# Optimization experiments

Hardware: AMD Instinct MI355X
Metric: run time of the kernel (lower is better)

The kernel has to match this reference:

```python
import jax, jax.numpy as jnp
import numpy as np

D_MODEL = 1024
N_HEADS = 16
D_HEAD = D_MODEL // N_HEADS
RANK = 16
DECAY = 0.95
ALPHA_MAX = 0.05
BETA = 0.01


def setup_inputs() -> dict:
    key = jax.random.key(0)
    ks = jax.random.split(key, 9)
    B, T = 4, 2048
    s = 0.02  # init scale for weights
    return {
        "hidden_states": jax.random.normal(ks[0], (B, T, D_MODEL), jnp.float32),
        "m_gate": jax.random.uniform(ks[1], (B, T), jnp.float32),
        "alpha_scale": jax.random.uniform(ks[2], (B, T, N_HEADS), jnp.float32),
        "Wq": jax.random.normal(ks[3], (D_MODEL, D_MODEL), jnp.float32) * s,
        "Wk": jax.random.normal(ks[4], (D_MODEL, D_MODEL), jnp.float32) * s,
        "Wv": jax.random.normal(ks[5], (D_MODEL, D_MODEL), jnp.float32) * s,
        "Wo": jax.random.normal(ks[6], (D_MODEL, D_MODEL), jnp.float32) * s,
        "Wa": jax.random.normal(ks[7], (N_HEADS, D_MODEL), jnp.float32) * s,
        "ba": jnp.zeros((N_HEADS,), jnp.float32),
        "mix_logit": jnp.zeros((N_HEADS,), jnp.float32),
    }


def reference(hidden_states, m_gate, alpha_scale, Wq, Wk, Wv, Wo, Wa, ba, mix_logit):
    B, T, D = hidden_states.shape
    H, Dh, R = N_HEADS, D_HEAD, RANK
    # batched projections (Linear: x @ W.T), then split heads
    q = (hidden_states @ Wq.T).reshape(B, T, H, Dh)
    k = (hidden_states @ Wk.T).reshape(B, T, H, Dh)
    v = (hidden_states @ Wv.T).reshape(B, T, H, Dh)
    # alpha computed under torch.no_grad in the original -> stop_gradient
    alpha = jax.nn.sigmoid(hidden_states @ Wa.T + ba)  # [B,T,H]
    alpha = alpha * m_gate[..., None] * alpha_scale
    alpha = jnp.minimum(alpha, ALPHA_MAX)
    alpha = jax.lax.stop_gradient(alpha)

    inv_sqrt_dh = 1.0 / (Dh ** 0.5)

    def step(carry, xs):
        U, V = carry  # U: [B,H,Dh,R], V: [B,H,R,Dh]
        q_t, k_t, v_t, a_t = xs  # [B,H,Dh], [B,H,Dh], [B,H,Dh], [B,H]
        U = DECAY * U
        V = DECAY * V
        ku = jnp.einsum('bhd,bhdr->bhr', k_t, U)
        a = a_t[..., None, None]
        U = U + a * jnp.einsum('bhd,bhr->bhdr', k_t, ku)
        V = V + a * jnp.einsum('bhr,bhd->bhrd', ku, v_t)
        U = U - BETA * jnp.clip(U, -1.0, 1.0)
        V = V - BETA * jnp.clip(V, -1.0, 1.0)
        # whole fast-weight update is no_grad in the original
        U = jax.lax.stop_gradient(U)
        V = jax.lax.stop_gradient(V)
        q_norm = q_t * inv_sqrt_dh
        k_fast = jnp.einsum('bhdr,bhrd->bhd', U, V)  # [B,H,Dh]
        score_slow = jnp.sum(q_norm * k_t, axis=-1)  # [B,H]
        score_fast = jnp.sum(q_norm * k_fast, axis=-1)
        logits = jnp.stack([score_slow, score_fast], axis=-1) + mix_logit[None, :, None]
        mix = jax.nn.softmax(logits, axis=-1)  # [B,H,2]
        y = mix[..., 0:1] * v_t + mix[..., 1:2] * k_fast  # [B,H,Dh]
        return (U, V), y

    U0 = jnp.zeros((B, H, Dh, R), hidden_states.dtype)
    V0 = jnp.zeros((B, H, R, Dh), hidden_states.dtype)
    xs = (jnp.moveaxis(q, 1, 0), jnp.moveaxis(k, 1, 0),
          jnp.moveaxis(v, 1, 0), jnp.moveaxis(alpha, 1, 0))
    _, ys = jax.lax.scan(step, (U0, V0), xs)  # ys: [T,B,H,Dh]
    y = jnp.moveaxis(ys, 0, 1).reshape(B, T, D)
    return y @ Wo.T
```

## Files before the change

kernel.cpp:

```cpp
#include <hip/hip_runtime.h>
#include <hip/hip_bf16.h>
#include <stdint.h>

#define D_MODEL 1024
#define N_HEADS 16
#define D_HEAD  64
#define SEQ_T   2048
#define BATCH   4

typedef unsigned short u16;
typedef __bf16 bf16x8 __attribute__((ext_vector_type(8)));
typedef float  f32x4  __attribute__((ext_vector_type(4)));

#define NT 32
#define BUF 4096
#define QNT 32

__device__ __forceinline__ u16 f2bf(float x) {
  unsigned u = __float_as_uint(x);
  u += 0x7fffu + ((u >> 16) & 1u);
  return (u16)(u >> 16);
}
__device__ __forceinline__ unsigned pk2(float a, float b) {
  return (unsigned)f2bf(a) | ((unsigned)f2bf(b) << 16);
}
__device__ __forceinline__ unsigned scale2(unsigned p, float s) {
  float lo = __uint_as_float(p << 16) * s;
  float hi = __uint_as_float(p & 0xffff0000u) * s;
  unsigned r;
  asm("v_cvt_pk_bf16_f32 %0, %1, %2" : "=v"(r) : "v"(lo), "v"(hi));
  return r;
}
__device__ __forceinline__ void cp16(const u16* g, u16* l) {
  __builtin_amdgcn_global_load_lds(
      (const __attribute__((address_space(1))) unsigned int*)g,
      (__attribute__((address_space(3))) unsigned int*)l, 16, 0, 0);
}

__global__ __launch_bounds__(256) void cast_kernel(const float* __restrict__ hs,
                                                   const float* __restrict__ wq,
                                                   const float* __restrict__ wk,
                                                   const float* __restrict__ wv,
                                                   const float* __restrict__ wo,
                                                   u16* __restrict__ Xb,
                                                   u16* __restrict__ Wb) {
  int g = blockIdx.x * 256 + threadIdx.x;
  const float4* src; uint4* dst;
  if (g < (1 << 20)) {
    src = (const float4*)hs + 2 * (size_t)g;
    dst = (uint4*)Xb + g;
  } else {
    int j = g - (1 << 20);
    int R = j >> 7;
    int col8 = j & 127;
    const float* s;
    int srow;
    if (R < 2048) {
      int h = R >> 7, c = R & 127, jj = c >> 4, l = c & 15;
      srow = h * 64 + (jj >> 1) * 16 + l;
      s = (jj & 1) ? wk : wq;
    } else if (R < 3072) { s = wv; srow = R - 2048; }
    else                 { s = wo; srow = R - 3072; }
    src = (const float4*)s + (size_t)srow * 256 + col8 * 2;
    dst = (uint4*)Wb + (size_t)R * 128 + col8;
  }
  float4 lo = src[0], hi = src[1];
  uint4 o;
  o.x = pk2(lo.x, lo.y); o.y = pk2(lo.z, lo.w);
  o.z = pk2(hi.x, hi.y); o.w = pk2(hi.z, hi.w);
  *dst = o;
}

#define QVM(n) asm volatile("s_waitcnt vmcnt(" #n ")" ::: "memory")

__global__ __launch_bounds__(256, 2) void gemm_qkv_kernel(const u16* __restrict__ A,
                                                          const u16* __restrict__ B,
                                                          u16* __restrict__ Vb,
                                                          float* __restrict__ S) {
  __shared__ u16 Ls[36864];
  const int tid  = threadIdx.x;
  const int w    = tid >> 6;
  const int l    = tid & 63;
  const int quad = l >> 4;
  const int l16  = l & 15;
  const int wm   = (w >> 1) * 128;
  const int wn   = (w & 1) * 64;

  const int id  = blockIdx.y * 24 + blockIdx.x;
  const int id2 = (id & 7) * 96 + (id >> 3);
  const int bm  = id2 / 24;
  const int bn  = id2 % 24;

  const int srow = w * 16 + (l >> 2);
  const int schk = (l & 3) * 8;
  const u16* aS[4]; const u16* bS[2];
  #pragma unroll
  for (int r = 0; r < 4; ++r)
    aS[r] = A + (size_t)(bm * 256 + r * 64 + srow) * 1024 + schk;
  #pragma unroll
  for (int r = 0; r < 2; ++r)
    bS[r] = B + (size_t)(bn * 128 + r * 64 + srow) * 1024 + schk;
  u16* dA = Ls + w * 512 + l * 8;
  u16* dB = Ls + 24576 + w * 512 + l * 8;

  f32x4 acc[8][4];
  #pragma unroll
  for (int i = 0; i < 8; ++i)
    #pragma unroll
    for (int j = 0; j < 4; ++j) acc[i][j] = (f32x4){0.f, 0.f, 0.f, 0.f};

  #pragma unroll
  for (int r = 0; r < 4; ++r) cp16(aS[r] + 0 * 32, dA + 0 * 8192 + r * 2048);
  #pragma unroll
  for (int r = 0; r < 2; ++r) cp16(bS[r] + 0 * 32, dB + 0 * 4096 + r * 2048);
  #pragma unroll
  for (int r = 0; r < 4; ++r) cp16(aS[r] + 1 * 32, dA + 1 * 8192 + r * 2048);
  #pragma unroll
  for (int r = 0; r < 2; ++r) cp16(bS[r] + 1 * 32, dB + 1 * 4096 + r * 2048);
  QVM(6);
  __builtin_amdgcn_s_barrier();

  int rbuf = 0, sbuf = 2;
  #pragma unroll 1
  for (int t = 0; t < QNT; ++t) {
    if (t + 2 < QNT) {
      #pragma unroll
      for (int r = 0; r < 4; ++r)
        cp16(aS[r] + (t + 2) * 32, dA + sbuf * 8192 + r * 2048);
      #pragma unroll
      for (int r = 0; r < 2; ++r)
        cp16(bS[r] + (t + 2) * 32, dB + sbuf * 4096 + r * 2048);
    }
    const u16* Ar = Ls + rbuf * 8192;
    const u16* Br = Ls + 24576 + rbuf * 4096;
    bf16x8 af[8], bfr[4];
    #pragma unroll
    for (int i = 0; i < 8; ++i)
      af[i] = *(const bf16x8*)(Ar + (wm + i * 16 + l16) * 32 + quad * 8);
    #pragma unroll
    for (int j = 0; j < 4; ++j)
      bfr[j] = *(const bf16x8*)(Br + (wn + j * 16 + l16) * 32 + quad * 8);
    __builtin_amdgcn_s_setprio(1);
    #pragma unroll
    for (int i = 0; i < 8; ++i)
      #pragma unroll
      for (int j = 0; j < 4; ++j)
        acc[i][j] = __builtin_amdgcn_mfma_f32_16x16x32_bf16(af[i], bfr[j], acc[i][j], 0, 0, 0);
    __builtin_amdgcn_s_setprio(0);
    if (t + 2 < QNT) { QVM(6); } else { QVM(0); }
    __builtin_amdgcn_s_barrier();
    rbuf = (rbuf == 2) ? 0 : rbuf + 1;
    sbuf = (sbuf == 2) ? 0 : sbuf + 1;
  }

  if (bn < 16) {
    float part[8][4];
    #pragma unroll
    for (int i = 0; i < 8; ++i)
      #pragma unroll
      for (int e = 0; e < 4; ++e)
        part[i][e] = acc[i][0][e] * acc[i][1][e] + acc[i][2][e] * acc[i][3][e];
    #pragma unroll
    for (int m = 1; m <= 8; m <<= 1)
      #pragma unroll
      for (int i = 0; i < 8; ++i)
        #pragma unroll
        for (int e = 0; e < 4; ++e)
          part[i][e] += __shfl_xor(part[i][e], m);
    float* Sp = (float*)Ls;
    if (l16 == 0) {
      #pragma unroll
      for (int i = 0; i < 8; ++i)
        #pragma unroll
        for (int e = 0; e < 4; ++e)
          Sp[(wm + i * 16 + quad * 4 + e) * 2 + (w & 1)] = part[i][e];
    }
    __syncthreads();
    {
      int row = tid;
      float s = (Sp[row * 2] + Sp[row * 2 + 1]) * 0.125f;
      S[(size_t)(bm * 256 + row) * N_HEADS + bn] = 1.f / (1.f + __expf(-s));
    }
  } else {
    const int cb = (bn - 16) * 128;
    #pragma unroll
    for (int i = 0; i < 8; ++i)
      #pragma unroll
      for (int j = 0; j < 4; ++j)
        #pragma unroll
        for (int e = 0; e < 4; ++e) {
          int row = bm * 256 + wm + i * 16 + quad * 4 + e;
          int col = cb + wn + j * 16 + l16;
          Vb[(size_t)row * D_MODEL + col] = f2bf(acc[i][j][e]);
        }
  }
}

__global__ __launch_bounds__(256, 4) void gemm_out_kernel(const u16* __restrict__ A,
                                                          const u16* __restrict__ B,
                                                          const float* __restrict__ S,
                                                          float* __restrict__ C) {
  constexpr int K = D_MODEL, N = D_MODEL;
  __shared__ u16 As[2 * BUF];
  __shared__ u16 Bs[2 * BUF];
  const int tid  = threadIdx.x;
  const int lane = tid & 63;
  const int wave = tid >> 6;
  const int wm = (wave >> 1) * 64;
  const int wn = (wave & 1) * 64;
  const int quad = lane >> 4;
  const int l16  = lane & 15;
  const int rchunk = quad ^ ((l16 >> 1) & 3);

  const int id  = blockIdx.y * 8 + blockIdx.x;
  const int id2 = (id & 7) * 64 + (id >> 3);
  const int bm = (id2 >> 3) * 128;
  const int bn = (id2 & 7) * 128;

  const int lr = tid >> 2;
  const int lch = tid & 3;
  const int wch = lch ^ ((lr >> 1) & 3);
  const u16* Ap0 = A + (size_t)(bm + lr) * K + lch * 8;
  const u16* Ap1 = Ap0 + (size_t)64 * K;
  u16* Aw0 = As + lr * 32 + wch * 8;
  u16* Aw1 = Aw0 + 64 * 32;
  const float* Sp0 = S + (size_t)(bm + lr) * N_HEADS;
  const float* Sp1 = Sp0 + (size_t)64 * N_HEADS;

  const int srow = lane >> 2;
  const int gch  = (lane & 3) ^ ((lane >> 3) & 3);
  const u16* Bg0 = B + (size_t)(bn + wave * 16 + srow) * K + gch * 8;
  const u16* Bg1 = Bg0 + (size_t)64 * K;
  u16* Bl = Bs + wave * 16 * 32 + lane * 8;

  f32x4 acc[4][4];
  #pragma unroll
  for (int i = 0; i < 4; ++i)
    #pragma unroll
    for (int j = 0; j < 4; ++j) acc[i][j] = (f32x4){0.f, 0.f, 0.f, 0.f};

  uint4 a0 = *(const uint4*)Ap0;
  uint4 a1 = *(const uint4*)Ap1;
  float rs0 = Sp0[0], rs1 = Sp1[0];
  cp16(Bg0, Bl);           cp16(Bg1, Bl + 64 * 32);
  {
    uint4 w0, w1;
    w0.x = scale2(a0.x, rs0); w0.y = scale2(a0.y, rs0);
    w0.z = scale2(a0.z, rs0); w0.w = scale2(a0.w, rs0);
    w1.x = scale2(a1.x, rs1); w1.y = scale2(a1.y, rs1);
    w1.z = scale2(a1.z, rs1); w1.w = scale2(a1.w, rs1);
    *(uint4*)Aw0 = w0; *(uint4*)Aw1 = w1;
  }
  a0 = *(const uint4*)(Ap0 + 32);
  a1 = *(const uint4*)(Ap1 + 32);
  __syncthreads();

  #pragma unroll 2
  for (int t = 0; t < NT; ++t) {
    const int p = t & 1;
    const u16* Ar = As + p * BUF;
    const u16* Br = Bs + p * BUF;
    bf16x8 af[4], bfr[4];
    #pragma unroll
    for (int i = 0; i < 4; ++i)
      af[i] = *(const bf16x8*)(Ar + (wm + i * 16 + l16) * 32 + rchunk * 8);
    #pragma unroll
    for (int j = 0; j < 4; ++j)
      bfr[j] = *(const bf16x8*)(Br + (wn + j * 16 + l16) * 32 + rchunk * 8);
    if (t + 1 < NT) {
      const int q = (p ^ 1) * BUF;
      cp16(Bg0 + (t + 1) * 32, Bl + q);
      cp16(Bg1 + (t + 1) * 32, Bl + q + 64 * 32);
      uint4 w0, w1;
      w0.x = scale2(a0.x, rs0); w0.y = scale2(a0.y, rs0);
      w0.z = scale2(a0.z, rs0); w0.w = scale2(a0.w, rs0);
      w1.x = scale2(a1.x, rs1); w1.y = scale2(a1.y, rs1);
      w1.z = scale2(a1.z, rs1); w1.w = scale2(a1.w, rs1);
      *(uint4*)(Aw0 + q) = w0; *(uint4*)(Aw1 + q) = w1;
      if (t + 2 < NT) {
        const int o = (t + 2) * 32;
        a0 = *(const uint4*)(Ap0 + o);
        a1 = *(const uint4*)(Ap1 + o);
        rs0 = Sp0[(t + 2) >> 1];
        rs1 = Sp1[(t + 2) >> 1];
      }
    }
    #pragma unroll
    for (int i = 0; i < 4; ++i)
      #pragma unroll
      for (int j = 0; j < 4; ++j)
        acc[i][j] = __builtin_amdgcn_mfma_f32_16x16x32_bf16(af[i], bfr[j], acc[i][j], 0, 0, 0);
    __syncthreads();
  }

  #pragma unroll
  for (int i = 0; i < 4; ++i)
    #pragma unroll
    for (int j = 0; j < 4; ++j)
      #pragma unroll
      for (int e = 0; e < 4; ++e) {
        int row = bm + wm + i * 16 + quad * 4 + e;
        int col = bn + wn + j * 16 + l16;
        C[(size_t)row * N + col] = acc[i][j][e];
      }
}

extern "C" void kernel_launch(void* const* d_in, const int* in_sizes, int n_in,
                              void* d_out, int out_size, void* d_ws, size_t ws_size,
                              hipStream_t stream) {
  const float* hs = (const float*)d_in[0];
  const float* Wq = (const float*)d_in[3];
  const float* Wk = (const float*)d_in[4];
  const float* Wv = (const float*)d_in[5];
  const float* Wo = (const float*)d_in[6];

  char* ws = (char*)d_ws;
  u16*  Xb = (u16*)ws;
  u16*  Wb = (u16*)(ws + (16u << 20));
  u16*  Vb = (u16*)(ws + (24u << 20));
  float* Sb = (float*)(ws + (40u << 20));
  float* out = (float*)d_out;

  cast_kernel<<<6144, 256, 0, stream>>>(hs, Wq, Wk, Wv, Wo, Xb, Wb);
  gemm_qkv_kernel<<<dim3(24, 32), 256, 0, stream>>>(Xb, Wb, Vb, Sb);
  gemm_out_kernel<<<dim3(8, 64), 256, 0, stream>>>(
      Vb, Wb + (size_t)3072 * D_MODEL, Sb, out);
}
```

Baseline: 189.6 us.

## Fuse fp32-to-bf16 cast of hidden states into QKV GEMM A-tile staging

Stops pre-casting the 8M-element hidden_states to bf16 in a separate pass. The QKV GEMM now loads fp32 A tiles into registers, converts them with v_cvt_pk_bf16_f32, and writes them to LDS one stage behind the loads, while B still uses direct global-to-LDS copies. This removes a full read/write of the activation and shrinks the cast kernel, but the GEMM reads twice as many A bytes (each A tile is re-read by 24 column blocks), uses more registers, and adds LDS write work to the main loop.

New measurement: 201.4 us. +6.3%, slower.

```diff
diff --git a/kernel.cpp b/kernel.cpp
--- a/kernel.cpp
+++ b/kernel.cpp
@@ -24,12 +24,15 @@
 __device__ __forceinline__ unsigned pk2(float a, float b) {
   return (unsigned)f2bf(a) | ((unsigned)f2bf(b) << 16);
 }
+__device__ __forceinline__ unsigned cvtpk(float lo, float hi) {
+  unsigned r;
+  asm("v_cvt_pk_bf16_f32 %0, %1, %2" : "=v"(r) : "v"(lo), "v"(hi));
+  return r;
+}
 __device__ __forceinline__ unsigned scale2(unsigned p, float s) {
   float lo = __uint_as_float(p << 16) * s;
   float hi = __uint_as_float(p & 0xffff0000u) * s;
-  unsigned r;
-  asm("v_cvt_pk_bf16_f32 %0, %1, %2" : "=v"(r) : "v"(lo), "v"(hi));
-  return r;
+  return cvtpk(lo, hi);
 }
 __device__ __forceinline__ void cp16(const u16* g, u16* l) {
   __builtin_amdgcn_global_load_lds(
@@ -37,33 +40,24 @@
       (__attribute__((address_space(3))) unsigned int*)l, 16, 0, 0);
 }
 
-__global__ __launch_bounds__(256) void cast_kernel(const float* __restrict__ hs,
-                                                   const float* __restrict__ wq,
+__global__ __launch_bounds__(256) void cast_kernel(const float* __restrict__ wq,
                                                    const float* __restrict__ wk,
                                                    const float* __restrict__ wv,
                                                    const float* __restrict__ wo,
-                                                   u16* __restrict__ Xb,
                                                    u16* __restrict__ Wb) {
-  int g = blockIdx.x * 256 + threadIdx.x;
-  const float4* src; uint4* dst;
-  if (g < (1 << 20)) {
-    src = (const float4*)hs + 2 * (size_t)g;
-    dst = (uint4*)Xb + g;
-  } else {
-    int j = g - (1 << 20);
-    int R = j >> 7;
-    int col8 = j & 127;
-    const float* s;
-    int srow;
-    if (R < 2048) {
-      int h = R >> 7, c = R & 127, jj = c >> 4, l = c & 15;
-      srow = h * 64 + (jj >> 1) * 16 + l;
-      s = (jj & 1) ? wk : wq;
-    } else if (R < 3072) { s = wv; srow = R - 2048; }
-    else                 { s = wo; srow = R - 3072; }
-    src = (const float4*)s + (size_t)srow * 256 + col8 * 2;
-    dst = (uint4*)Wb + (size_t)R * 128 + col8;
-  }
+  int j = blockIdx.x * 256 + threadIdx.x;
+  int R = j >> 7;
+  int col8 = j & 127;
+  const float* s;
+  int srow;
+  if (R < 2048) {
+    int h = R >> 7, c = R & 127, jj = c >> 4, l = c & 15;
+    srow = h * 64 + (jj >> 1) * 16 + l;
+    s = (jj & 1) ? wk : wq;
+  } else if (R < 3072) { s = wv; srow = R - 2048; }
+  else                 { s = wo; srow = R - 3072; }
+  const float4* src = (const float4*)s + (size_t)srow * 256 + col8 * 2;
+  uint4* dst = (uint4*)Wb + (size_t)R * 128 + col8;
   float4 lo = src[0], hi = src[1];
   uint4 o;
   o.x = pk2(lo.x, lo.y); o.y = pk2(lo.z, lo.w);
@@ -73,7 +67,7 @@
 
 #define QVM(n) asm volatile("s_waitcnt vmcnt(" #n ")" ::: "memory")
 
-__global__ __launch_bounds__(256, 2) void gemm_qkv_kernel(const u16* __restrict__ A,
+__global__ __launch_bounds__(256, 2) void gemm_qkv_kernel(const float* __restrict__ A32,
                                                           const u16* __restrict__ B,
                                                           u16* __restrict__ Vb,
                                                           float* __restrict__ S) {
@@ -91,45 +85,69 @@
   const int bm  = id2 / 24;
   const int bn  = id2 % 24;
 
+  const int c4 = tid & 3;
+  const int r0 = tid >> 2;
+  const float* aG[4];
+  #pragma unroll
+  for (int u = 0; u < 4; ++u)
+    aG[u] = A32 + (size_t)(bm * 256 + u * 64 + r0) * 1024 + c4 * 8;
+  u16* aW = Ls + r0 * 32 + c4 * 8;
+
   const int srow = w * 16 + (l >> 2);
   const int schk = (l & 3) * 8;
-  const u16* aS[4]; const u16* bS[2];
-  #pragma unroll
-  for (int r = 0; r < 4; ++r)
-    aS[r] = A + (size_t)(bm * 256 + r * 64 + srow) * 1024 + schk;
+  const u16* bS[2];
   #pragma unroll
   for (int r = 0; r < 2; ++r)
     bS[r] = B + (size_t)(bn * 128 + r * 64 + srow) * 1024 + schk;
-  u16* dA = Ls + w * 512 + l * 8;
   u16* dB = Ls + 24576 + w * 512 + l * 8;
 
+  float4 av[4][2];
+
+#define STAGE_A_LOAD(t)                                                        \
+  do {                                                                         \
+    _Pragma("unroll") for (int _u = 0; _u < 4; ++_u) {                         \
+      av[_u][0] = *(const float4*)(aG[_u] + (t) * 32);                         \
+      av[_u][1] = *(const float4*)(aG[_u] + (t) * 32 + 4);                     \
+    }                                                                          \
+  } while (0)
+#define STAGE_A_WRITE(slot)                                                    \
+  do {                                                                         \
+    _Pragma("unroll") for (int _u = 0; _u < 4; ++_u) {                         \
+      uint4 _o;                                                                \
+      _o.x = cvtpk(av[_u][0].x, av[_u][0].y);                                  \
+      _o.y = cvtpk(av[_u][0].z, av[_u][0].w);                                  \
+      _o.z = cvtpk(av[_u][1].x, av[_u][1].y);                                  \
+      _o.w = cvtpk(av[_u][1].z, av[_u][1].w);                                  \
+      *(uint4*)(aW + (slot) * 8192 + _u * 2048) = _o;                          \
+    }                                                                          \
+  } while (0)
+#define STAGE_B(t, slot)                                                       \
+  do {                                                                         \
+    cp16(bS[0] + (t) * 32, dB + (slot) * 4096);                                \
+    cp16(bS[1] + (t) * 32, dB + (slot) * 4096 + 2048);                         \
+  } while (0)
+
   f32x4 acc[8][4];
   #pragma unroll
   for (int i = 0; i < 8; ++i)
     #pragma unroll
     for (int j = 0; j < 4; ++j) acc[i][j] = (f32x4){0.f, 0.f, 0.f, 0.f};
 
-  #pragma unroll
-  for (int r = 0; r < 4; ++r) cp16(aS[r] + 0 * 32, dA + 0 * 8192 + r * 2048);
-  #pragma unroll
-  for (int r = 0; r < 2; ++r) cp16(bS[r] + 0 * 32, dB + 0 * 4096 + r * 2048);
-  #pragma unroll
-  for (int r = 0; r < 4; ++r) cp16(aS[r] + 1 * 32, dA + 1 * 8192 + r * 2048);
-  #pragma unroll
-  for (int r = 0; r < 2; ++r) cp16(bS[r] + 1 * 32, dB + 1 * 4096 + r * 2048);
-  QVM(6);
+  STAGE_A_LOAD(0);
+  STAGE_B(0, 0);
+  STAGE_A_WRITE(0);
+  STAGE_A_LOAD(1);
+  STAGE_B(1, 1);
+  QVM(10);
   __builtin_amdgcn_s_barrier();
 
-  int rbuf = 0, sbuf = 2;
+  int rbuf = 0, wbuf = 1, sbuf = 2;
   #pragma unroll 1
   for (int t = 0; t < QNT; ++t) {
+    if (t + 1 < QNT) STAGE_A_WRITE(wbuf);
     if (t + 2 < QNT) {
-      #pragma unroll
-      for (int r = 0; r < 4; ++r)
-        cp16(aS[r] + (t + 2) * 32, dA + sbuf * 8192 + r * 2048);
-      #pragma unroll
-      for (int r = 0; r < 2; ++r)
-        cp16(bS[r] + (t + 2) * 32, dB + sbuf * 4096 + r * 2048);
+      STAGE_A_LOAD(t + 2);
+      STAGE_B(t + 2, sbuf);
     }
     const u16* Ar = Ls + rbuf * 8192;
     const u16* Br = Ls + 24576 + rbuf * 4096;
@@ -147,9 +165,11 @@
       for (int j = 0; j < 4; ++j)
         acc[i][j] = __builtin_amdgcn_mfma_f32_16x16x32_bf16(af[i], bfr[j], acc[i][j], 0, 0, 0);
     __builtin_amdgcn_s_setprio(0);
-    if (t + 2 < QNT) { QVM(6); } else { QVM(0); }
+    if (t + 2 < QNT) { QVM(10); }
+    else if (t + 1 < QNT) { QVM(0); }
     __builtin_amdgcn_s_barrier();
     rbuf = (rbuf == 2) ? 0 : rbuf + 1;
+    wbuf = (wbuf == 2) ? 0 : wbuf + 1;
     sbuf = (sbuf == 2) ? 0 : sbuf + 1;
   }
 
@@ -315,14 +335,13 @@
   const float* Wo = (const float*)d_in[6];
 
   char* ws = (char*)d_ws;
-  u16*  Xb = (u16*)ws;
-  u16*  Wb = (u16*)(ws + (16u << 20));
-  u16*  Vb = (u16*)(ws + (24u << 20));
-  float* Sb = (float*)(ws + (40u << 20));
+  u16*  Wb = (u16*)ws;
+  u16*  Vb = (u16*)(ws + (8u << 20));
+  float* Sb = (float*)(ws + (24u << 20));
   float* out = (float*)d_out;
 
-  cast_kernel<<<6144, 256, 0, stream>>>(hs, Wq, Wk, Wv, Wo, Xb, Wb);
-  gemm_qkv_kernel<<<dim3(24, 32), 256, 0, stream>>>(Xb, Wb, Vb, Sb);
+  cast_kernel<<<2048, 256, 0, stream>>>(Wq, Wk, Wv, Wo, Wb);
+  gemm_qkv_kernel<<<dim3(24, 32), 256, 0, stream>>>(hs, Wb, Vb, Sb);
   gemm_out_kernel<<<dim3(8, 64), 256, 0, stream>>>(
       Vb, Wb + (size_t)3072 * D_MODEL, Sb, out);
 }
```

## Apply per-head output scale to MFMA partials instead of rescaling A tiles

Applied to the files above, without the earlier changes.

The output GEMM no longer rescales each bf16 A element by the per-row, per-head mix weight before writing it to LDS. It now loads both A and B tiles straight into LDS asynchronously, with K=64 per stage (one head per stage). Each head's raw partial product is computed in a temporary accumulator and multiplied by the row scale in fp32 before being added to the main accumulator. This drops the VALU rescale and bf16 repack on the load path and avoids a second rounding of the scaled value. The cost is extra FMAs per element per stage, more registers, and a launch-bounds occupancy hint lowered from 4 to 2.

Result: no change. 186.6 us (-1.6%).

```diff
diff --git a/kernel.cpp b/kernel.cpp
--- a/kernel.cpp
+++ b/kernel.cpp
@@ -12,8 +12,6 @@
 typedef __bf16 bf16x8 __attribute__((ext_vector_type(8)));
 typedef float  f32x4  __attribute__((ext_vector_type(4)));
 
-#define NT 32
-#define BUF 4096
 #define QNT 32
 
 __device__ __forceinline__ u16 f2bf(float x) {
@@ -23,13 +21,6 @@
 }
 __device__ __forceinline__ unsigned pk2(float a, float b) {
   return (unsigned)f2bf(a) | ((unsigned)f2bf(b) << 16);
-}
-__device__ __forceinline__ unsigned scale2(unsigned p, float s) {
-  float lo = __uint_as_float(p << 16) * s;
-  float hi = __uint_as_float(p & 0xffff0000u) * s;
-  unsigned r;
-  asm("v_cvt_pk_bf16_f32 %0, %1, %2" : "=v"(r) : "v"(lo), "v"(hi));
-  return r;
 }
 __device__ __forceinline__ void cp16(const u16* g, u16* l) {
   __builtin_amdgcn_global_load_lds(
@@ -196,101 +187,109 @@
   }
 }
 
-__global__ __launch_bounds__(256, 4) void gemm_out_kernel(const u16* __restrict__ A,
+__global__ __launch_bounds__(256, 2) void gemm_out_kernel(const u16* __restrict__ A,
                                                           const u16* __restrict__ B,
                                                           const float* __restrict__ S,
                                                           float* __restrict__ C) {
-  constexpr int K = D_MODEL, N = D_MODEL;
-  __shared__ u16 As[2 * BUF];
-  __shared__ u16 Bs[2 * BUF];
+  constexpr int N = D_MODEL;
+  __shared__ u16 Ls[32768];
   const int tid  = threadIdx.x;
-  const int lane = tid & 63;
-  const int wave = tid >> 6;
-  const int wm = (wave >> 1) * 64;
-  const int wn = (wave & 1) * 64;
-  const int quad = lane >> 4;
-  const int l16  = lane & 15;
-  const int rchunk = quad ^ ((l16 >> 1) & 3);
+  const int l    = tid & 63;
+  const int w    = tid >> 6;
+  const int quad = l >> 4;
+  const int l16  = l & 15;
+  const int wm   = (w >> 1) * 64;
+  const int wn   = (w & 1) * 64;
 
   const int id  = blockIdx.y * 8 + blockIdx.x;
   const int id2 = (id & 7) * 64 + (id >> 3);
-  const int bm = (id2 >> 3) * 128;
-  const int bn = (id2 & 7) * 128;
-
-  const int lr = tid >> 2;
-  const int lch = tid & 3;
-  const int wch = lch ^ ((lr >> 1) & 3);
-  const u16* Ap0 = A + (size_t)(bm + lr) * K + lch * 8;
-  const u16* Ap1 = Ap0 + (size_t)64 * K;
-  u16* Aw0 = As + lr * 32 + wch * 8;
-  u16* Aw1 = Aw0 + 64 * 32;
-  const float* Sp0 = S + (size_t)(bm + lr) * N_HEADS;
-  const float* Sp1 = Sp0 + (size_t)64 * N_HEADS;
-
-  const int srow = lane >> 2;
-  const int gch  = (lane & 3) ^ ((lane >> 3) & 3);
-  const u16* Bg0 = B + (size_t)(bn + wave * 16 + srow) * K + gch * 8;
-  const u16* Bg1 = Bg0 + (size_t)64 * K;
-  u16* Bl = Bs + wave * 16 * 32 + lane * 8;
+  const int bm  = (id2 >> 3) * 128;
+  const int bn  = (id2 & 7) * 128;
+
+  const int srow = tid >> 3;
+  const int sch  = ((tid & 7) ^ (srow & 7)) * 8;
+  const u16* aG[4]; const u16* bG[4];
+  #pragma unroll
+  for (int u = 0; u < 4; ++u) {
+    aG[u] = A + (size_t)(bm + u * 32 + srow) * 1024 + sch;
+    bG[u] = B + (size_t)(bn + u * 32 + srow) * 1024 + sch;
+  }
+  u16* dA = Ls + tid * 8;
+  u16* dB = Ls + 16384 + tid * 8;
+
+#define OSTAGE(t, b)                                                           \
+  do {                                                                         \
+    _Pragma("unroll") for (int _u = 0; _u < 4; ++_u) {                         \
+      cp16(aG[_u] + (t) * 64, dA + (b) * 8192 + _u * 2048);                    \
+      cp16(bG[_u] + (t) * 64, dB + (b) * 8192 + _u * 2048);                    \
+    }                                                                          \
+  } while (0)
+
+  const int rc0 = ((0 + quad) ^ (l16 & 7)) * 8;
+  const int rc1 = ((4 + quad) ^ (l16 & 7)) * 8;
+
+  const float* Srow[4];
+  #pragma unroll
+  for (int i = 0; i < 4; ++i)
+    Srow[i] = S + (size_t)(bm + wm + i * 16 + quad * 4) * N_HEADS;
 
   f32x4 acc[4][4];
   #pragma unroll
   for (int i = 0; i < 4; ++i)
     #pragma unroll
     for (int j = 0; j < 4; ++j) acc[i][j] = (f32x4){0.f, 0.f, 0.f, 0.f};
-
-  uint4 a0 = *(const uint4*)Ap0;
-  uint4 a1 = *(const uint4*)Ap1;
-  float rs0 = Sp0[0], rs1 = Sp1[0];
-  cp16(Bg0, Bl);           cp16(Bg1, Bl + 64 * 32);
-  {
-    uint4 w0, w1;
-    w0.x = scale2(a0.x, rs0); w0.y = scale2(a0.y, rs0);
-    w0.z = scale2(a0.z, rs0); w0.w = scale2(a0.w, rs0);
-    w1.x = scale2(a1.x, rs1); w1.y = scale2(a1.y, rs1);
-    w1.z = scale2(a1.z, rs1); w1.w = scale2(a1.w, rs1);
-    *(uint4*)Aw0 = w0; *(uint4*)Aw1 = w1;
-  }
-  a0 = *(const uint4*)(Ap0 + 32);
-  a1 = *(const uint4*)(Ap1 + 32);
-  __syncthreads();
-
-  #pragma unroll 2
-  for (int t = 0; t < NT; ++t) {
-    const int p = t & 1;
-    const u16* Ar = As + p * BUF;
-    const u16* Br = Bs + p * BUF;
-    bf16x8 af[4], bfr[4];
+  const f32x4 z4 = (f32x4){0.f, 0.f, 0.f, 0.f};
+
+  OSTAGE(0, 0);
+  QVM(0);
+  __builtin_amdgcn_s_barrier();
+
+  #pragma unroll 1
+  for (int t = 0; t < 16; ++t) {
+    float sv[4][4];
     #pragma unroll
     for (int i = 0; i < 4; ++i)
-      af[i] = *(const bf16x8*)(Ar + (wm + i * 16 + l16) * 32 + rchunk * 8);
-    #pragma unroll
-    for (int j = 0; j < 4; ++j)
-      bfr[j] = *(const bf16x8*)(Br + (wn + j * 16 + l16) * 32 + rchunk * 8);
-    if (t + 1 < NT) {
-      const int q = (p ^ 1) * BUF;
-      cp16(Bg0 + (t + 1) * 32, Bl + q);
-      cp16(Bg1 + (t + 1) * 32, Bl + q + 64 * 32);
-      uint4 w0, w1;
-      w0.x = scale2(a0.x, rs0); w0.y = scale2(a0.y, rs0);
-      w0.z = scale2(a0.z, rs0); w0.w = scale2(a0.w, rs0);
-      w1.x = scale2(a1.x, rs1); w1.y = scale2(a1.y, rs1);
-      w1.z = scale2(a1.z, rs1); w1.w = scale2(a1.w, rs1);
-      *(uint4*)(Aw0 + q) = w0; *(uint4*)(Aw1 + q) = w1;
-      if (t + 2 < NT) {
-        const int o = (t + 2) * 32;
-        a0 = *(const uint4*)(Ap0 + o);
-        a1 = *(const uint4*)(Ap1 + o);
-        rs0 = Sp0[(t + 2) >> 1];
-        rs1 = Sp1[(t + 2) >> 1];
-      }
-    }
-    #pragma unroll
-    for (int i = 0; i < 4; ++i)
-      #pragma unroll
-      for (int j = 0; j < 4; ++j)
-        acc[i][j] = __builtin_amdgcn_mfma_f32_16x16x32_bf16(af[i], bfr[j], acc[i][j], 0, 0, 0);
-    __syncthreads();
+      #pragma unroll
+      for (int e = 0; e < 4; ++e)
+        sv[i][e] = Srow[i][e * N_HEADS + t];
+    if (t + 1 < 16) OSTAGE(t + 1, (t + 1) & 1);
+    const u16* Ar = Ls + (t & 1) * 8192;
+    const u16* Br = Ls + 16384 + (t & 1) * 8192;
+    bf16x8 af[2][4], bfr[2][4];
+    #pragma unroll
+    for (int i = 0; i < 4; ++i) {
+      af[0][i]  = *(const bf16x8*)(Ar + (wm + i * 16 + l16) * 64 + rc0);
+      af[1][i]  = *(const bf16x8*)(Ar + (wm + i * 16 + l16) * 64 + rc1);
+      bfr[0][i] = *(const bf16x8*)(Br + (wn + i * 16 + l16) * 64 + rc0);
+      bfr[1][i] = *(const bf16x8*)(Br + (wn + i * 16 + l16) * 64 + rc1);
+    }
+    __builtin_amdgcn_s_setprio(1);
+    #pragma unroll
+    for (int jh = 0; jh < 2; ++jh) {
+      f32x4 pacc[4][2];
+      #pragma unroll
+      for (int i = 0; i < 4; ++i)
+        #pragma unroll
+        for (int jj = 0; jj < 2; ++jj)
+          pacc[i][jj] = __builtin_amdgcn_mfma_f32_16x16x32_bf16(
+              af[0][i], bfr[0][jh * 2 + jj], z4, 0, 0, 0);
+      #pragma unroll
+      for (int i = 0; i < 4; ++i)
+        #pragma unroll
+        for (int jj = 0; jj < 2; ++jj)
+          pacc[i][jj] = __builtin_amdgcn_mfma_f32_16x16x32_bf16(
+              af[1][i], bfr[1][jh * 2 + jj], pacc[i][jj], 0, 0, 0);
+      #pragma unroll
+      for (int i = 0; i < 4; ++i)
+        #pragma unroll
+        for (int jj = 0; jj < 2; ++jj)
+          #pragma unroll
+          for (int e = 0; e < 4; ++e)
+            acc[i][jh * 2 + jj][e] += sv[i][e] * pacc[i][jj][e];
+    }
+    __builtin_amdgcn_s_setprio(0);
+    QVM(0);
+    __builtin_amdgcn_s_barrier();
   }
 
   #pragma unroll
```
